# Optimization experiments

Measured on AMD Instinct MI355X. Metric: run time of the kernel, lower is better.

## Reference

```python
import jax, jax.numpy as jnp
import numpy as np

B, S, E, H, Dh = 4, 2048, 2048, 16, 128
EPS = 1e-6

def rms_norm(x, scale):
    # RMSNorm over last dim (the module calls it LayerNorm but uses mean of squares)
    x = x.astype(jnp.float32)
    mean2 = jnp.mean(jnp.square(x), axis=-1, keepdims=True)
    return (x * jax.lax.rsqrt(mean2 + EPS)) * scale

def setup_inputs() -> dict:
    key = jax.random.key(0)
    ks = jax.random.split(key, 8)
    sd = 1.0 / np.sqrt(E)
    Wq = jax.random.normal(ks[0], (E, H, Dh), jnp.float32) * sd / np.sqrt(Dh)  # query_init divides by sqrt(head_dim)
    Wk = jax.random.normal(ks[1], (E, H, Dh), jnp.float32) * sd
    Wv = jax.random.normal(ks[2], (E, H, Dh), jnp.float32) * sd
    Wo = jax.random.normal(ks[3], (H, Dh, E), jnp.float32) * (1.0 / np.sqrt(H * Dh))
    return {
        "inputs_q": jax.random.normal(ks[4], (B, S, E), jnp.float32),
        "inputs_kv": jax.random.normal(ks[5], (B, S, E), jnp.float32),
        "Wq": Wq, "Wk": Wk, "Wv": Wv,
        "q_ln_scale": jnp.ones((Dh,), jnp.float32),
        "k_ln_scale": jnp.ones((Dh,), jnp.float32),
        "Wo": Wo,
    }

def reference(inputs_q, inputs_kv, Wq, Wk, Wv, q_ln_scale, k_ln_scale, Wo):
    # QKV projections: [B,S,E] x [E,H,Dh] -> [B,S,H,Dh]
    q = jnp.einsum('bqe,ehd->bqhd', inputs_q, Wq)
    k = jnp.einsum('bke,ehd->bkhd', inputs_kv, Wk)
    v = jnp.einsum('bke,ehd->bkhd', inputs_kv, Wv)
    # QK RMS-norm before attention (the non-standard fusion-defeating step)
    q = rms_norm(q, q_ln_scale)
    k = rms_norm(k, k_ln_scale)
    # attention logits and softmax (no mask/bias, deterministic)
    logits = jnp.einsum('bqhd,bkhd->bhqk', q, k)
    probs = jax.nn.softmax(logits, axis=-1)
    # weighted values and output projection
    ctx = jnp.einsum('bhqk,bkhd->bqhd', probs, v)
    out = jnp.einsum('bqhd,hde->bqe', ctx, Wo)
    return out
```

## Files before the change

kernel.cpp:

```cpp
#include <hip/hip_runtime.h>
#include <hip/hip_bf16.h>

typedef unsigned short u16;
typedef unsigned int u32;
typedef _Float16 f16;
typedef __attribute__((ext_vector_type(8))) short bf16x8;
typedef __attribute__((ext_vector_type(8))) _Float16 f16x8;
typedef __attribute__((ext_vector_type(4))) float f32x4;
typedef __attribute__((ext_vector_type(4))) u16 u16x4;

__device__ __forceinline__ float bf2f(u16 u){ return __uint_as_float(((u32)u) << 16); }
__device__ __forceinline__ u16 f2bf(float f){
  u32 u = __float_as_uint(f);
  u += 0x7fffu + ((u >> 16) & 1u);
  return (u16)(u >> 16);
}
__device__ __forceinline__ void gll16(const u16* g, u16* l){
  __builtin_amdgcn_global_load_lds((const __attribute__((address_space(1))) u32*)g,
                                   (__attribute__((address_space(3))) u32*)l, 16, 0, 0);
}

#define MFMA16(a,b,c) __builtin_amdgcn_mfma_f32_16x16x32_bf16((a),(b),(c),0,0,0)
#define MFMAH(a,b,c)  __builtin_amdgcn_mfma_f32_16x16x32_f16((a),(b),(c),0,0,0)

__global__ __launch_bounds__(256) void cvt_f16(const float* __restrict__ in, u16* __restrict__ out){
  const size_t i = ((size_t)blockIdx.x*256 + threadIdx.x)*8;
  f16 h[8];
  #pragma unroll
  for (int j=0;j<8;j++) h[j] = (f16)in[i+j];
  *(f16x8*)(out+i) = *(f16x8*)h;
}

__global__ __launch_bounds__(256) void transpose_w(const float* __restrict__ in, u16* __restrict__ oh){
  __shared__ float tile[64*68];
  const int t = threadIdx.x;
  const int r0 = blockIdx.y*64, c0 = blockIdx.x*64;
  #pragma unroll
  for (int p=0;p<2;p++){
    const int row = p*32 + (t>>3), cg = (t&7)*8;
    const float* s = in + (size_t)(r0+row)*2048 + c0 + cg;
    #pragma unroll
    for (int j=0;j<8;j++) tile[row*68 + cg + j] = s[j];
  }
  __syncthreads();
  #pragma unroll
  for (int p=0;p<2;p++){
    const int orow = p*32 + (t>>3), cg = (t&7)*8;
    f16 h[8];
    #pragma unroll
    for (int j=0;j<8;j++) h[j] = (f16)(tile[(cg+j)*68 + orow] * 256.f);
    *(f16x8*)(oh + (size_t)(c0+orow)*2048 + r0 + cg) = *(f16x8*)h;
  }
}

template<int EPI>
__global__ __launch_bounds__(512, 1) void gemm8(const u16* __restrict__ A,
                                                const u16* __restrict__ Bt,
                                                const float* __restrict__ scale,
                                                u16* __restrict__ C,
                                                float* __restrict__ Cf){
  constexpr int K = 2048, NT = 32;
  __shared__ __align__(16) u16 AL[2][2][8192];
  __shared__ __align__(16) u16 BL[2][2][8192];
  __shared__ float red[2][4][128];

  const int t = threadIdx.x;
  const int lane = t & 63, w = t >> 6;
  const int wm = w >> 2, wn = w & 3;
  const int l15 = lane & 15, l4 = lane >> 4;

  const int bid = blockIdx.x;
  const int xcd = bid & 7, q = bid >> 3;
  const int m0 = (((xcd >> 1) << 3) + (q >> 2)) * 256;
  const int n0 = (((xcd & 1) << 2) + (q & 3)) * 256;

  const int srow = t >> 2;
  const int skg = (t & 3) ^ ((srow ^ (srow >> 2)) & 3);
  const u16* gA = A  + (size_t)(m0 + srow) * K + skg * 8;
  const u16* gB = Bt + (size_t)(n0 + srow) * K + skg * 8;
  const int d0 = (w * 64) * 8;
  const int d1 = (512 + w * 64) * 8;

  const int sz = (l15 ^ (l15 >> 2)) & 3;
  const int kgp = ((l4 ^ sz) & 3) * 8;
  const int aoff = (wm * 128 + l15) * 32 + kgp;
  const int boff = (wn * 64 + l15) * 32 + kgp;

  f32x4 acc[8][4] = {};

#define STG_A(tile, kh, db) { const u16* s_ = gA + (size_t)(tile)*64 + (kh)*32; \
    gll16(s_, &AL[db][kh][0] + d0); gll16(s_ + (size_t)128*K, &AL[db][kh][0] + d1); }
#define STG_B(tile, kh, db) { const u16* s_ = gB + (size_t)(tile)*64 + (kh)*32; \
    gll16(s_, &BL[db][kh][0] + d0); gll16(s_ + (size_t)128*K, &BL[db][kh][0] + d1); }

  STG_A(0,0,0); STG_B(0,0,0);
  STG_A(0,1,0); STG_B(0,1,0);
  STG_A(1,0,1); STG_B(1,0,1);
  asm volatile("s_waitcnt vmcnt(4)" ::: "memory");
  __builtin_amdgcn_s_barrier();

  for (int g = 0; g < NT; ++g){
    const int db = g & 1, db1 = db ^ 1;
    const int t1 = (g+1 < NT) ? g+1 : NT-1;
    const int t2 = (g+2 < NT) ? g+2 : NT-1;
    f16x8 a[4], b[4];

    #pragma unroll
    for (int nf=0; nf<4; nf++) b[nf] = *(const f16x8*)&BL[db][0][boff + nf*512];
    #pragma unroll
    for (int mf=0; mf<4; mf++) a[mf] = *(const f16x8*)&AL[db][0][aoff + mf*512];
    STG_A(t1, 1, db1);
    __builtin_amdgcn_s_barrier();
    asm volatile("s_waitcnt lgkmcnt(0)" ::: "memory");
    __builtin_amdgcn_sched_barrier(0);
    __builtin_amdgcn_s_setprio(1);
    #pragma unroll
    for (int mf=0; mf<4; mf++)
      #pragma unroll
      for (int nf=0; nf<4; nf++)
        acc[mf][nf] = MFMAH(a[mf], b[nf], acc[mf][nf]);
    __builtin_amdgcn_s_setprio(0);
    __builtin_amdgcn_s_barrier();

    #pragma unroll
    for (int mf=0; mf<4; mf++) a[mf] = *(const f16x8*)&AL[db][0][aoff + (mf+4)*512];
    STG_B(t1, 1, db1);
    __builtin_amdgcn_s_barrier();
    asm volatile("s_waitcnt lgkmcnt(0)" ::: "memory");
    __builtin_amdgcn_sched_barrier(0);
    __builtin_amdgcn_s_setprio(1);
    #pragma unroll
    for (int mf=0; mf<4; mf++)
      #pragma unroll
      for (int nf=0; nf<4; nf++)
        acc[mf+4][nf] = MFMAH(a[mf], b[nf], acc[mf+4][nf]);
    __builtin_amdgcn_s_setprio(0);
    __builtin_amdgcn_s_barrier();

    #pragma unroll
    for (int nf=0; nf<4; nf++) b[nf] = *(const f16x8*)&BL[db][1][boff + nf*512];
    #pragma unroll
    for (int mf=0; mf<4; mf++) a[mf] = *(const f16x8*)&AL[db][1][aoff + mf*512];
    STG_A(t2, 0, db);
    __builtin_amdgcn_s_barrier();
    asm volatile("s_waitcnt lgkmcnt(0)" ::: "memory");
    __builtin_amdgcn_sched_barrier(0);
    __builtin_amdgcn_s_setprio(1);
    #pragma unroll
    for (int mf=0; mf<4; mf++)
      #pragma unroll
      for (int nf=0; nf<4; nf++)
        acc[mf][nf] = MFMAH(a[mf], b[nf], acc[mf][nf]);
    __builtin_amdgcn_s_setprio(0);
    __builtin_amdgcn_s_barrier();

    #pragma unroll
    for (int mf=0; mf<4; mf++) a[mf] = *(const f16x8*)&AL[db][1][aoff + (mf+4)*512];
    STG_B(t2, 0, db);
    __builtin_amdgcn_s_barrier();
    asm volatile("s_waitcnt lgkmcnt(0)" ::: "memory");
    __builtin_amdgcn_sched_barrier(0);
    __builtin_amdgcn_s_setprio(1);
    #pragma unroll
    for (int mf=0; mf<4; mf++)
      #pragma unroll
      for (int nf=0; nf<4; nf++)
        acc[mf+4][nf] = MFMAH(a[mf], b[nf], acc[mf+4][nf]);
    __builtin_amdgcn_s_setprio(0);
    asm volatile("s_waitcnt vmcnt(4)" ::: "memory");
    __builtin_amdgcn_s_barrier();
  }

  asm volatile("s_waitcnt vmcnt(0)" ::: "memory");
  __builtin_amdgcn_s_barrier();

  const float us = 1.f/256.f;
  if (EPI == 0){
    #pragma unroll
    for (int mf=0; mf<8; mf++)
      #pragma unroll
      for (int nf=0; nf<4; nf++)
        #pragma unroll
        for (int r=0;r<4;r++) acc[mf][nf][r] *= us;
    #pragma unroll
    for (int mf=0; mf<8; mf++){
      #pragma unroll
      for (int r=0;r<4;r++){
        float p = acc[mf][0][r]*acc[mf][0][r] + acc[mf][1][r]*acc[mf][1][r]
                + acc[mf][2][r]*acc[mf][2][r] + acc[mf][3][r]*acc[mf][3][r];
        #pragma unroll
        for (int d=1; d<16; d<<=1) p += __shfl_xor(p, d, 64);
        if (l15 == 0) red[wm][wn][mf*16 + l4*4 + r] = p;
      }
    }
    __syncthreads();
    float sc[4];
    #pragma unroll
    for (int nf=0; nf<4; nf++) sc[nf] = scale[(wn*64 + nf*16 + l15) & 127];
    #pragma unroll
    for (int mf=0; mf<8; mf++){
      #pragma unroll
      for (int r=0;r<4;r++){
        const int rl = mf*16 + l4*4 + r;
        const float inv = rsqrtf((red[wm][wn & 2][rl] + red[wm][(wn & 2) | 1][rl])*(1.f/128.f) + 1e-6f);
        const size_t grow = (size_t)(m0 + wm*128 + rl);
        #pragma unroll
        for (int nf=0; nf<4; nf++){
          f16 hv = (f16)(acc[mf][nf][r]*inv*sc[nf]);
          C[grow*2048 + (n0 + wn*64 + nf*16 + l15)] = *reinterpret_cast<u16*>(&hv);
        }
      }
    }
  } else if (EPI == 1){
    #pragma unroll
    for (int mf=0; mf<8; mf++){
      const int m = m0 + wm*128 + mf*16 + l4*4;
      const int bb = m >> 11, s = m & 2047;
      #pragma unroll
      for (int nf=0; nf<4; nf++){
        const int n = n0 + wn*64 + nf*16 + l15;
        u16x4 pk;
        pk.x = f2bf(acc[mf][nf][0]*us); pk.y = f2bf(acc[mf][nf][1]*us);
        pk.z = f2bf(acc[mf][nf][2]*us); pk.w = f2bf(acc[mf][nf][3]*us);
        *(u16x4*)&C[((size_t)(bb*16 + (n>>7))*128 + (n&127))*2048 + s] = pk;
      }
    }
  } else {
    #pragma unroll
    for (int mf=0; mf<8; mf++){
      const size_t r0 = (size_t)(m0 + wm*128 + mf*16 + l4*4);
      #pragma unroll
      for (int nf=0; nf<4; nf++){
        const int c = n0 + wn*64 + nf*16 + l15;
        #pragma unroll
        for (int r=0;r<4;r++)
          Cf[(r0+r)*2048 + c] = acc[mf][nf][r]*us;
      }
    }
  }
#undef STG_A
#undef STG_B
}

__global__ __launch_bounds__(256, 3) void attn_fwd(const u16* __restrict__ Qh_,
                                                   const u16* __restrict__ Kh_,
                                                   const u16* __restrict__ Vt, u16* __restrict__ O){
  __shared__ __align__(16) u16 Ksh[64*128];
  __shared__ __align__(16) u16 Vsh[128*64];
  __shared__ __align__(16) u16 Psh[4][32*72];
  const int t = threadIdx.x;
  const int lane = t & 63, w = t >> 6;
  const int l15 = lane & 15, l4 = lane >> 4;
  const int lin = blockIdx.x;
  const int bh  = (lin & 7)*8 + (lin >> 7);
  const int qt  = (lin >> 3) & 15;
  const int b = bh >> 4, h = bh & 15;
  const int q0 = qt*128 + w*32;

  f16x8 qh[2][4];
  #pragma unroll
  for (int qf=0;qf<2;qf++){
    const size_t qoff = ((size_t)((b<<11) + q0 + qf*16 + l15)*16 + h)*128 + l4*8;
    #pragma unroll
    for (int kk=0;kk<4;kk++)
      qh[qf][kk] = *(const f16x8*)(Qh_ + qoff + kk*32);
  }
  f32x4 oacc[2][8] = {};
  float lpart[2][4] = {};

  size_t ksrc[4], vsrc[4];
  #pragma unroll
  for (int p=0;p<4;p++){
    const int g = p*256 + t;
    ksrc[p] = ((size_t)((b<<11) + (g>>4))*16 + h)*128 + (size_t)((((g&15) ^ ((g>>4)&7))*8));
    vsrc[p] = ((size_t)(b*16 + h)*128 + (g>>3))*2048 + (size_t)((((g&7) ^ ((g>>3)&7))*8));
  }

  for (int kt = 0; kt < 2048; kt += 64){
    __syncthreads();
    const size_t ko = (size_t)kt*2048;
    #pragma unroll
    for (int p=0;p<4;p++){
      const int g = p*256 + t;
      gll16(Kh_ + ksrc[p] + ko, Ksh + g*8);
      gll16(Vt + vsrc[p] + kt, Vsh + g*8);
    }
    __syncthreads();

    f32x4 sa[2][4] = {};
    #pragma unroll
    for (int ks=0;ks<4;ks++){
      const int row = ks*16 + l15;
      #pragma unroll
      for (int kk=0;kk<4;kk++){
        const int off = row*128 + (((kk*4 + l4) ^ (row&7))*8);
        f16x8 khf = *(const f16x8*)&Ksh[off];
        sa[0][ks] = MFMAH(qh[0][kk], khf, sa[0][ks]);
        sa[1][ks] = MFMAH(qh[1][kk], khf, sa[1][ks]);
      }
    }
    #pragma unroll
    for (int qf=0;qf<2;qf++)
      #pragma unroll
      for (int r=0;r<4;r++){
        float rs = 0.f;
        #pragma unroll
        for (int ks=0;ks<4;ks++){
          const float e = __expf(sa[qf][ks][r] - 24.f);
          rs += e;
          Psh[w][(qf*16 + l4*4 + r)*72 + ks*16 + l15] = f2bf(e);
        }
        lpart[qf][r] += rs;
      }
    asm volatile("s_waitcnt lgkmcnt(0)" ::: "memory");
    __builtin_amdgcn_sched_barrier(0);

    #pragma unroll
    for (int ks2=0;ks2<2;ks2++){
      bf16x8 pa0 = *(const bf16x8*)&Psh[w][(l15)*72 + ks2*32 + l4*8];
      bf16x8 pa1 = *(const bf16x8*)&Psh[w][(16 + l15)*72 + ks2*32 + l4*8];
      #pragma unroll
      for (int n=0;n<8;n++){
        const int row = n*16 + l15;
        const int c8 = ks2*4 + l4;
        bf16x8 vb = *(const bf16x8*)&Vsh[row*64 + ((c8 ^ (row&7))*8)];
        oacc[0][n] = MFMA16(pa0, vb, oacc[0][n]);
        oacc[1][n] = MFMA16(pa1, vb, oacc[1][n]);
      }
    }
  }

  #pragma unroll
  for (int qf=0;qf<2;qf++){
    float lrun[4];
    #pragma unroll
    for (int r=0;r<4;r++){
      float s = lpart[qf][r];
      #pragma unroll
      for (int d=1; d<16; d<<=1) s += __shfl_xor(s, d, 64);
      lrun[r] = s;
    }
    #pragma unroll
    for (int n=0;n<8;n++){
      const int d = n*16 + l15;
      #pragma unroll
      for (int r=0;r<4;r++){
        const int s = q0 + qf*16 + l4*4 + r;
        f16 hv = (f16)(oacc[qf][n][r] / lrun[r]);
        O[((size_t)((b<<11) + s)*16 + h)*128 + d] = *reinterpret_cast<u16*>(&hv);
      }
    }
  }
}

extern "C" void kernel_launch(void* const* d_in, const int* in_sizes, int n_in,
                              void* d_out, int out_size, void* d_ws, size_t ws_size,
                              hipStream_t stream){
  const float* f_inq = (const float*)d_in[0];
  const float* f_inkv= (const float*)d_in[1];
  const float* f_Wq  = (const float*)d_in[2];
  const float* f_Wk  = (const float*)d_in[3];
  const float* f_Wv  = (const float*)d_in[4];
  const float* scq   = (const float*)d_in[5];
  const float* sck   = (const float*)d_in[6];
  const float* f_Wo  = (const float*)d_in[7];

  u16* ws = (u16*)d_ws;
  const size_t ACT = (size_t)16777216;
  const size_t WEL = (size_t)4194304;
  u16* q_h = ws;
  u16* k_h = q_h + ACT;
  u16* v_t = k_h + ACT;
  u16* ctx = v_t + ACT;
  u16* wq  = ctx + ACT;
  u16* wk  = wq + WEL;
  u16* wv  = wk + WEL;
  u16* wo  = wv + WEL;

  u16* inq16  = (u16*)d_out;
  u16* inkv16 = inq16 + ACT;

  cvt_f16<<<8192, 256, 0, stream>>>(f_inq,  inq16);
  cvt_f16<<<8192, 256, 0, stream>>>(f_inkv, inkv16);

  dim3 tg(32,32);
  transpose_w<<<tg, 256, 0, stream>>>(f_Wq, wq);
  transpose_w<<<tg, 256, 0, stream>>>(f_Wk, wk);
  transpose_w<<<tg, 256, 0, stream>>>(f_Wv, wv);
  transpose_w<<<tg, 256, 0, stream>>>(f_Wo, wo);

  gemm8<0><<<256, 512, 0, stream>>>(inq16,  wq, scq, q_h, nullptr);
  gemm8<0><<<256, 512, 0, stream>>>(inkv16, wk, sck, k_h, nullptr);
  gemm8<1><<<256, 512, 0, stream>>>(inkv16, wv, nullptr, v_t, nullptr);

  attn_fwd<<<dim3(1024), 256, 0, stream>>>(q_h, k_h, v_t, ctx);

  gemm8<2><<<256, 512, 0, stream>>>(ctx, wo, nullptr, nullptr, (float*)d_out);
}
```

Before: 554.0 us.

## Double-buffer K tiles and prefetch V/K asynchronously in attention loop

Restructures the attention K/V loading into a software pipeline. K is double-buffered in LDS and prefetched two tiles ahead, while V is prefetched one tile ahead, with vmcnt-based waits and raw s_barriers replacing the full syncthreads pairs. The aim is to hide global-to-LDS load latency behind the QK and PV MFMA work. It raises LDS use and lowers the occupancy hint from 3 to 2 blocks per CU, and it depends on hand-counted vmcnt values, which are fragile.

```diff
diff --git a/kernel.cpp b/kernel.cpp
--- a/kernel.cpp
+++ b/kernel.cpp
@@ -242,10 +242,10 @@
 #undef STG_B
 }
 
-__global__ __launch_bounds__(256, 3) void attn_fwd(const u16* __restrict__ Qh_,
+__global__ __launch_bounds__(256, 2) void attn_fwd(const u16* __restrict__ Qh_,
                                                    const u16* __restrict__ Kh_,
                                                    const u16* __restrict__ Vt, u16* __restrict__ O){
-  __shared__ __align__(16) u16 Ksh[64*128];
+  __shared__ __align__(16) u16 Ksh[2][64*128];
   __shared__ __align__(16) u16 Vsh[128*64];
   __shared__ __align__(16) u16 Psh[4][32*72];
   const int t = threadIdx.x;
@@ -276,16 +276,17 @@
     vsrc[p] = ((size_t)(b*16 + h)*128 + (g>>3))*2048 + (size_t)((((g&7) ^ ((g>>3)&7))*8));
   }
 
-  for (int kt = 0; kt < 2048; kt += 64){
-    __syncthreads();
-    const size_t ko = (size_t)kt*2048;
-    #pragma unroll
-    for (int p=0;p<4;p++){
-      const int g = p*256 + t;
-      gll16(Kh_ + ksrc[p] + ko, Ksh + g*8);
-      gll16(Vt + vsrc[p] + kt, Vsh + g*8);
-    }
-    __syncthreads();
+#define STK(T, DB) { const size_t ko_ = (size_t)(T)*131072; \
+    _Pragma("unroll") for (int p_=0;p_<4;p_++) gll16(Kh_ + ksrc[p_] + ko_, &Ksh[DB][0] + (p_*256+t)*8); }
+#define STV(T) { const int vo_ = (T)*64; \
+    _Pragma("unroll") for (int p_=0;p_<4;p_++) gll16(Vt + vsrc[p_] + vo_, &Vsh[0] + (p_*256+t)*8); }
+
+  STK(0,0); STV(0); STK(1,1);
+  asm volatile("s_waitcnt vmcnt(4)" ::: "memory");
+  __builtin_amdgcn_s_barrier();
+
+  for (int tt = 0; tt < 32; ++tt){
+    const int c = tt & 1;
 
     f32x4 sa[2][4] = {};
     #pragma unroll
@@ -294,7 +295,7 @@
       #pragma unroll
       for (int kk=0;kk<4;kk++){
         const int off = row*128 + (((kk*4 + l4) ^ (row&7))*8);
-        f16x8 khf = *(const f16x8*)&Ksh[off];
+        f16x8 khf = *(const f16x8*)&Ksh[c][off];
         sa[0][ks] = MFMAH(qh[0][kk], khf, sa[0][ks]);
         sa[1][ks] = MFMAH(qh[1][kk], khf, sa[1][ks]);
       }
@@ -312,8 +313,9 @@
         }
         lpart[qf][r] += rs;
       }
-    asm volatile("s_waitcnt lgkmcnt(0)" ::: "memory");
+    asm volatile("s_waitcnt vmcnt(4) lgkmcnt(0)" ::: "memory");
     __builtin_amdgcn_sched_barrier(0);
+    __builtin_amdgcn_s_barrier();
 
     #pragma unroll
     for (int ks2=0;ks2<2;ks2++){
@@ -328,7 +330,18 @@
         oacc[1][n] = MFMA16(pa1, vb, oacc[1][n]);
       }
     }
-  }
+    __builtin_amdgcn_s_barrier();
+
+    const int tv = (tt+1 < 32) ? tt+1 : 31;
+    const int tk = (tt+2 < 32) ? tt+2 : 31;
+    STV(tv); STK(tk, c);
+    asm volatile("s_waitcnt vmcnt(8)" ::: "memory");
+    __builtin_amdgcn_s_barrier();
+  }
+  asm volatile("s_waitcnt vmcnt(0)" ::: "memory");
+
+#undef STK
+#undef STV
 
   #pragma unroll
   for (int qf=0;qf<2;qf++){
```

Measured after the change: 533.7 us. 1.04x faster.
